# Optimization experiments

Hardware: AMD Instinct MI355X
Metric: run time of the kernel (lower is better)

## Reference

```python
import jax, jax.numpy as jnp
import numpy as np

EMBED = 512
HEADS = 8
SEQ = 2048
HD = EMBED // HEADS  # 64
N_BATCH = 2


def setup_inputs() -> dict:
    key = jax.random.key(0)
    ks = jax.random.split(key, 15)
    f = jax.random.normal
    return {
        "v": f(ks[0], (N_BATCH, SEQ, EMBED), jnp.float32),
        "k": f(ks[1], (N_BATCH, SEQ, EMBED), jnp.float32),
        "q": f(ks[2], (N_BATCH, SEQ, EMBED), jnp.float32),
        # per-head Linear(head_dim, head_dim) weights (stored torch-style [out,in]) + biases
        "Wv": f(ks[3], (HD, HD), jnp.float32) * (HD ** -0.5),
        "bv": f(ks[4], (HD,), jnp.float32) * 0.01,
        "Wk": f(ks[5], (HD, HD), jnp.float32) * (HD ** -0.5),
        "bk": f(ks[6], (HD,), jnp.float32) * 0.01,
        "Wq": f(ks[7], (HD, HD), jnp.float32) * (HD ** -0.5),
        "bq": f(ks[8], (HD,), jnp.float32) * 0.01,
        # relative position embedding E: [1, seq_len, head_dim]
        "E": f(ks[9], (1, SEQ, HD), jnp.float32),
        # fc_out Linear(embed, embed)
        "Wo": f(ks[10], (EMBED, EMBED), jnp.float32) * (EMBED ** -0.5),
        "bo": f(ks[11], (EMBED,), jnp.float32) * 0.01,
    }


def reference(v, k, q, Wv, bv, Wk, bk, Wq, bq, E, Wo, bo):
    N, S, Emb = v.shape
    H = HEADS
    Hd = Emb // H
    # split heads then per-head projections (Linear acts on last dim head_dim)
    values = v.reshape(N, S, H, Hd) @ Wv.T + bv   # [N,S,H,Hd]
    keys = k.reshape(N, S, H, Hd) @ Wk.T + bk
    queries = q.reshape(N, S, H, Hd) @ Wq.T + bq

    # --- Music-Transformer relative-position skew ---
    # QE = queries.transpose(1,2) @ E.transpose(1,2): [N,H,S,Hd] x [Hd,S] -> [N,H,S,S]
    QE = jnp.einsum('nshd,ld->nhsl', queries, E[0])
    triu1 = jnp.triu(jnp.ones((S, S), dtype=jnp.float32), 1)
    pos_mask = jnp.flip(triu1, axis=1)            # triu(...,1).flip(1)
    QE = jnp.where(pos_mask == 1, 0.0, QE)        # _mask_positions
    padded = jnp.pad(QE, ((0, 0), (0, 0), (0, 0), (1, 0)))  # F.pad(qe, [1,0])
    Srel = padded.reshape(N, H, S + 1, S)[:, :, 1:, :]       # _skew -> [N,H,S,S]

    # --- scores + mask (faithful to original: masked_fill(mask==0, -1e20)
    # i.e. lower triangle incl. diagonal gets -1e20) ---
    qk = jnp.einsum('nqhd,nkhd->nhqk', queries, keys)
    qk = jnp.where(triu1[None, None] == 0, jnp.float32(-1e20), qk)

    # note: scaled by sqrt(embed_size), as in the source
    attention = jax.nn.softmax(qk / jnp.sqrt(jnp.float32(Emb)), axis=3) + Srel

    z = jnp.einsum('nhql,nlhd->nqhd', attention, values).reshape(N, S, H * Hd)
    return z @ Wo.T + bo
```

## Files before the change

kernel.cpp:

```cpp
#include <hip/hip_runtime.h>
#include <hip/hip_bf16.h>

#define SEQLEN 2048
#define NHEADS 8
#define HD 64
#define EMB 512
#define NB 2
#define ST 72

typedef __attribute__((ext_vector_type(8))) short bf16x8;
typedef __attribute__((ext_vector_type(4))) float f32x4;

#define SCALE 0.04419417382415922f
#define NEGS  (-4.4194173824159216e18f)

__device__ __forceinline__ ushort f2b(float f) {
    __hip_bfloat16 h = __float2bfloat16(f);
    return *reinterpret_cast<ushort*>(&h);
}
__device__ __forceinline__ float b2f(ushort u) {
    unsigned int v = ((unsigned int)u) << 16;
    return __builtin_bit_cast(float, v);
}
__device__ __forceinline__ uint4 pack8(float4 a, float4 b) {
    union { ushort u[8]; uint4 v; } r;
    r.u[0] = f2b(a.x); r.u[1] = f2b(a.y); r.u[2] = f2b(a.z); r.u[3] = f2b(a.w);
    r.u[4] = f2b(b.x); r.u[5] = f2b(b.y); r.u[6] = f2b(b.z); r.u[7] = f2b(b.w);
    return r.v;
}

__global__ __launch_bounds__(256, 4) void proj_mfma(
    const float* __restrict__ q, const float* __restrict__ k, const float* __restrict__ v,
    const float* __restrict__ Wq, const float* __restrict__ bq,
    const float* __restrict__ Wk, const float* __restrict__ bk,
    const float* __restrict__ Wv, const float* __restrict__ bv,
    ushort* __restrict__ Qh, ushort* __restrict__ Kh, ushort* __restrict__ VT)
{
    const int mat = blockIdx.z;
    const float* x; const float* W; const float* b;
    switch (mat) {
      case 0:  x = q; W = Wq; b = bq; break;
      case 1:  x = k; W = Wk; b = bk; break;
      default: x = v; W = Wv; b = bv; break;
    }
    __shared__ alignas(16) ushort At[64 * ST];
    __shared__ alignas(16) ushort Bt[64 * ST];
    __shared__ alignas(16) ushort Ct[64 * ST];

    const int tid = threadIdx.x;
    const int w = tid >> 6, l = tid & 63;
    const int l15 = l & 15, l16 = l >> 4;
    const int h  = blockIdx.y;
    const int m0 = blockIdx.x * 64;
    const int n  = m0 / SEQLEN;
    const int s0 = m0 - n * SEQLEN;
    const int wm = (w >> 1) * 32, wn = (w & 1) * 32;
    const int r8 = tid >> 3, ch8 = (tid & 7) * 8;

    {
        const float* xr0 = x + (size_t)(m0 + r8) * EMB + h * HD + ch8;
        const float* xr1 = x + (size_t)(m0 + r8 + 32) * EMB + h * HD + ch8;
        float4 a0 = *(const float4*)xr0, a1 = *(const float4*)(xr0 + 4);
        float4 a2 = *(const float4*)xr1, a3 = *(const float4*)(xr1 + 4);
        const float* wr0 = W + r8 * HD + ch8;
        const float* wr1 = W + (r8 + 32) * HD + ch8;
        float4 b0 = *(const float4*)wr0, b1 = *(const float4*)(wr0 + 4);
        float4 b2 = *(const float4*)wr1, b3 = *(const float4*)(wr1 + 4);
        *(uint4*)&At[r8 * ST + ch8]        = pack8(a0, a1);
        *(uint4*)&At[(r8 + 32) * ST + ch8] = pack8(a2, a3);
        *(uint4*)&Bt[r8 * ST + ch8]        = pack8(b0, b1);
        *(uint4*)&Bt[(r8 + 32) * ST + ch8] = pack8(b2, b3);
    }
    __syncthreads();

    f32x4 acc[2][2];
    #pragma unroll
    for (int i = 0; i < 2; ++i)
        #pragma unroll
        for (int j = 0; j < 2; ++j) acc[i][j] = (f32x4){0.f, 0.f, 0.f, 0.f};

    #pragma unroll
    for (int ks = 0; ks < 2; ++ks) {
        const int ko = ks * 32 + l16 * 8;
        bf16x8 af[2], bf[2];
        #pragma unroll
        for (int i = 0; i < 2; ++i) {
            af[i] = *(const bf16x8*)&At[(wm + i * 16 + l15) * ST + ko];
            bf[i] = *(const bf16x8*)&Bt[(wn + i * 16 + l15) * ST + ko];
        }
        #pragma unroll
        for (int i = 0; i < 2; ++i)
            #pragma unroll
            for (int j = 0; j < 2; ++j)
                acc[i][j] = __builtin_amdgcn_mfma_f32_16x16x32_bf16(af[i], bf[j], acc[i][j], 0, 0, 0);
    }

    float bb[2];
    #pragma unroll
    for (int j = 0; j < 2; ++j) bb[j] = b[wn + j * 16 + l15];
    #pragma unroll
    for (int i = 0; i < 2; ++i)
        #pragma unroll
        for (int j = 0; j < 2; ++j)
            #pragma unroll
            for (int r = 0; r < 4; ++r) {
                const int srow = wm + i * 16 + l16 * 4 + r;
                const int dcol = wn + j * 16 + l15;
                const ushort val = f2b(acc[i][j][r] + bb[j]);
                if (mat < 2) Ct[srow * ST + dcol] = val;
                else         Ct[dcol * ST + srow] = val;
            }
    __syncthreads();

    const size_t hb = ((size_t)(n * NHEADS + h)) * SEQLEN * HD;
    if (mat < 2) {
        ushort* dst = (mat == 0 ? Qh : Kh);
        *(uint4*)(dst + hb + (size_t)(s0 + r8) * HD + ch8)      = *(uint4*)&Ct[r8 * ST + ch8];
        *(uint4*)(dst + hb + (size_t)(s0 + r8 + 32) * HD + ch8) = *(uint4*)&Ct[(r8 + 32) * ST + ch8];
    } else {
        *(uint4*)(VT + hb + (size_t)r8 * SEQLEN + s0 + ch8)        = *(uint4*)&Ct[r8 * ST + ch8];
        *(uint4*)(VT + hb + (size_t)(r8 + 32) * SEQLEN + s0 + ch8) = *(uint4*)&Ct[(r8 + 32) * ST + ch8];
    }
}

__global__ __launch_bounds__(256) void econv_kernel(
    const float* __restrict__ E, ushort* __restrict__ Eb)
{
    const int i = (blockIdx.x * 256 + threadIdx.x) * 4;
    float4 f = *(const float4*)(E + i);
    ushort4 u;
    u.x = f2b(f.x); u.y = f2b(f.y); u.z = f2b(f.z); u.w = f2b(f.w);
    *(ushort4*)(Eb + i) = u;
}

__global__ __launch_bounds__(256, 2) void attn_mfma(
    const ushort* __restrict__ Qh, const ushort* __restrict__ Kh,
    const ushort* __restrict__ VT, const ushort* __restrict__ Eb,
    ushort* __restrict__ Z)
{
    const int q0 = blockIdx.x * 64;
    const int h = blockIdx.y, n = blockIdx.z;
    const int tid = threadIdx.x;
    const int w = tid >> 6;
    const int l = tid & 63;
    const int l15 = l & 15, l16 = l >> 4;

    __shared__ alignas(16) ushort Kt[64 * ST];
    __shared__ alignas(16) ushort Vt[64 * ST];
    __shared__ alignas(16) ushort Et[128 * ST];
    __shared__ alignas(16) ushort Wt[4][16 * ST];
    __shared__ float vpart[4][64];
    __shared__ float vsum[64];

    const size_t hb = ((size_t)(n * NHEADS + h)) * SEQLEN * HD;
    const bool lastBlk = (q0 == SEQLEN - 64);
    const int qw = q0 + 16 * w;

    bf16x8 qa[2];
    {
        const ushort* qp = Qh + hb + (size_t)(qw + l15) * HD + l16 * 8;
        qa[0] = *(const bf16x8*)(qp);
        qa[1] = *(const bf16x8*)(qp + 32);
    }

    f32x4 zp[4], zr[4];
    #pragma unroll
    for (int nb = 0; nb < 4; ++nb) {
        zp[nb] = (f32x4){0.f, 0.f, 0.f, 0.f};
        zr[nb] = (f32x4){0.f, 0.f, 0.f, 0.f};
    }
    float mrow[4], lrow[4];
    #pragma unroll
    for (int r = 0; r < 4; ++r) { mrow[r] = NEGS; lrow[r] = 0.f; }
    float vloc = 0.f;

    for (int t = 0; t < 32; ++t) {
        const int c0 = t * 64;
        const bool hasP = (c0 >= q0);
        const bool hasR = (c0 <= q0);
        const bool diag = (c0 == q0);

        __syncthreads();
        {
            const int r8 = tid >> 3;
            const int ch8 = (tid & 7) * 8;
            uint4 v0 = *(const uint4*)(VT + hb + (size_t)r8 * SEQLEN + c0 + ch8);
            uint4 v1 = *(const uint4*)(VT + hb + (size_t)(r8 + 32) * SEQLEN + c0 + ch8);
            uint4 k0, k1;
            if (hasP) {
                k0 = *(const uint4*)(Kh + hb + (size_t)(c0 + r8) * HD + ch8);
                k1 = *(const uint4*)(Kh + hb + (size_t)(c0 + r8 + 32) * HD + ch8);
            }
            uint4 e[4];
            int jmin = 0;
            if (hasR) {
                jmin = SEQLEN - 64 - q0 + c0;
                #pragma unroll
                for (int i = 0; i < 4; ++i) {
                    const int j = jmin + r8 + 32 * i;
                    if (j < SEQLEN) e[i] = *(const uint4*)(Eb + (size_t)j * HD + ch8);
                    else e[i] = make_uint4(0u, 0u, 0u, 0u);
                }
            }
            *(uint4*)&Vt[r8 * ST + ch8] = v0;
            *(uint4*)&Vt[(r8 + 32) * ST + ch8] = v1;
            if (hasP) {
                *(uint4*)&Kt[r8 * ST + ch8] = k0;
                *(uint4*)&Kt[(r8 + 32) * ST + ch8] = k1;
            }
            if (hasR) {
                #pragma unroll
                for (int i = 0; i < 4; ++i)
                    *(uint4*)&Et[(r8 + 32 * i) * ST + ch8] = e[i];
            }
        }
        __syncthreads();

        if (lastBlk) {
            const uint4 a = *(const uint4*)&Vt[l * ST + 16 * w];
            const uint4 b = *(const uint4*)&Vt[l * ST + 16 * w + 8];
            const ushort* pa = (const ushort*)&a;
            const ushort* pb = (const ushort*)&b;
            #pragma unroll
            for (int i = 0; i < 8; ++i) vloc += b2f(pa[i]) + b2f(pb[i]);
        }

        if (hasP) {
            f32x4 sc[4];
            #pragma unroll
            for (int nb = 0; nb < 4; ++nb) sc[nb] = (f32x4){0.f, 0.f, 0.f, 0.f};
            #pragma unroll
            for (int ks = 0; ks < 2; ++ks) {
                const int ko = ks * 32 + l16 * 8;
                #pragma unroll
                for (int nb = 0; nb < 4; ++nb) {
                    bf16x8 kb = *(const bf16x8*)&Kt[(nb * 16 + l15) * ST + ko];
                    sc[nb] = __builtin_amdgcn_mfma_f32_16x16x32_bf16(qa[ks], kb, sc[nb], 0, 0, 0);
                }
            }
            float sv[4][4], mt[4], frs[4];
            #pragma unroll
            for (int r = 0; r < 4; ++r) mt[r] = NEGS;
            #pragma unroll
            for (int nb = 0; nb < 4; ++nb)
                #pragma unroll
                for (int r = 0; r < 4; ++r) {
                    float s = sc[nb][r] * SCALE;
                    if (diag && (nb * 16 + l15 <= 16 * w + l16 * 4 + r)) s = NEGS;
                    sv[nb][r] = s;
                    mt[r] = fmaxf(mt[r], s);
                }
            #pragma unroll
            for (int r = 0; r < 4; ++r) {
                #pragma unroll
                for (int off = 1; off < 16; off <<= 1)
                    mt[r] = fmaxf(mt[r], __shfl_xor(mt[r], off, 64));
                const float mn = fmaxf(mrow[r], mt[r]);
                frs[r] = __expf(mrow[r] - mn);
                mrow[r] = mn;
                lrow[r] *= frs[r];
            }
            float se[4] = {0.f, 0.f, 0.f, 0.f};
            #pragma unroll
            for (int nb = 0; nb < 4; ++nb)
                #pragma unroll
                for (int r = 0; r < 4; ++r) {
                    const float e = __expf(sv[nb][r] - mrow[r]);
                    se[r] += e;
                    Wt[w][(l16 * 4 + r) * ST + nb * 16 + l15] = f2b(e);
                }
            #pragma unroll
            for (int r = 0; r < 4; ++r) {
                #pragma unroll
                for (int off = 1; off < 16; off <<= 1)
                    se[r] += __shfl_xor(se[r], off, 64);
                lrow[r] += se[r];
            }
            #pragma unroll
            for (int nb = 0; nb < 4; ++nb)
                #pragma unroll
                for (int r = 0; r < 4; ++r) zp[nb][r] *= frs[r];
            #pragma unroll
            for (int ks = 0; ks < 2; ++ks) {
                const int ko = ks * 32 + l16 * 8;
                bf16x8 wa = *(const bf16x8*)&Wt[w][l15 * ST + ko];
                #pragma unroll
                for (int nb = 0; nb < 4; ++nb) {
                    bf16x8 vb = *(const bf16x8*)&Vt[(nb * 16 + l15) * ST + ko];
                    zp[nb] = __builtin_amdgcn_mfma_f32_16x16x32_bf16(wa, vb, zp[nb], 0, 0, 0);
                }
            }
        }

        if (hasR) {
            const int jbase = 48 - 16 * w;
            f32x4 qe[5];
            #pragma unroll
            for (int jb = 0; jb < 5; ++jb) qe[jb] = (f32x4){0.f, 0.f, 0.f, 0.f};
            #pragma unroll
            for (int ks = 0; ks < 2; ++ks) {
                const int ko = ks * 32 + l16 * 8;
                #pragma unroll
                for (int jb = 0; jb < 5; ++jb) {
                    bf16x8 eb = *(const bf16x8*)&Et[(jbase + jb * 16 + l15) * ST + ko];
                    qe[jb] = __builtin_amdgcn_mfma_f32_16x16x32_bf16(qa[ks], eb, qe[jb], 0, 0, 0);
                }
            }
            #pragma unroll
            for (int jb = 0; jb < 5; ++jb)
                #pragma unroll
                for (int r = 0; r < 4; ++r) {
                    const int rowloc = l16 * 4 + r;
                    const int cloc = jb * 16 + l15 + rowloc - 15;
                    if (cloc >= 0 && cloc < 64) {
                        const bool msk = (c0 + cloc <= qw + rowloc);
                        Wt[w][rowloc * ST + cloc] = f2b(msk ? qe[jb][r] : 0.f);
                    }
                }
            #pragma unroll
            for (int ks = 0; ks < 2; ++ks) {
                const int ko = ks * 32 + l16 * 8;
                bf16x8 wa = *(const bf16x8*)&Wt[w][l15 * ST + ko];
                #pragma unroll
                for (int nb = 0; nb < 4; ++nb) {
                    bf16x8 vb = *(const bf16x8*)&Vt[(nb * 16 + l15) * ST + ko];
                    zr[nb] = __builtin_amdgcn_mfma_f32_16x16x32_bf16(wa, vb, zr[nb], 0, 0, 0);
                }
            }
        }
    }

    if (lastBlk) vpart[w][l] = vloc;
    __syncthreads();
    if (lastBlk && tid < 64)
        vsum[tid] = vpart[0][tid] + vpart[1][tid] + vpart[2][tid] + vpart[3][tid];
    __syncthreads();

    float invl[4];
    #pragma unroll
    for (int r = 0; r < 4; ++r) invl[r] = 1.f / lrow[r];
    #pragma unroll
    for (int nb = 0; nb < 4; ++nb)
        #pragma unroll
        for (int r = 0; r < 4; ++r) {
            const int q = qw + l16 * 4 + r;
            const int d = nb * 16 + l15;
            float z = zp[nb][r] * invl[r] + zr[nb][r];
            if (lastBlk && q == SEQLEN - 1)
                z = vsum[d] * (1.f / (float)SEQLEN) + zr[nb][r];
            Z[((size_t)(n * SEQLEN + q)) * EMB + h * HD + d] = f2b(z);
        }
}

__global__ __launch_bounds__(256, 4) void oproj_mfma(
    const ushort* __restrict__ Zb, const ushort* __restrict__ Wob,
    const float* __restrict__ bo, float* __restrict__ out)
{
    __shared__ alignas(16) ushort At[64 * ST];
    __shared__ alignas(16) ushort Bt[64 * ST];
    const int tid = threadIdx.x;
    const int w = tid >> 6, l = tid & 63;
    const int l15 = l & 15, l16 = l >> 4;
    const int m0 = blockIdx.x * 64;
    const int n0 = blockIdx.y * 64;
    const int wm = (w >> 1) * 32, wn = (w & 1) * 32;
    const int r8 = tid >> 3, ch8 = (tid & 7) * 8;

    f32x4 acc[2][2];
    #pragma unroll
    for (int i = 0; i < 2; ++i)
        #pragma unroll
        for (int j = 0; j < 2; ++j) acc[i][j] = (f32x4){0.f, 0.f, 0.f, 0.f};

    for (int kt = 0; kt < 8; ++kt) {
        const int k0 = kt * 64;
        __syncthreads();
        {
            uint4 a0 = *(const uint4*)(Zb  + (size_t)(m0 + r8) * EMB + k0 + ch8);
            uint4 a1 = *(const uint4*)(Zb  + (size_t)(m0 + r8 + 32) * EMB + k0 + ch8);
            uint4 b0 = *(const uint4*)(Wob + (size_t)(n0 + r8) * EMB + k0 + ch8);
            uint4 b1 = *(const uint4*)(Wob + (size_t)(n0 + r8 + 32) * EMB + k0 + ch8);
            *(uint4*)&At[r8 * ST + ch8] = a0;
            *(uint4*)&At[(r8 + 32) * ST + ch8] = a1;
            *(uint4*)&Bt[r8 * ST + ch8] = b0;
            *(uint4*)&Bt[(r8 + 32) * ST + ch8] = b1;
        }
        __syncthreads();
        #pragma unroll
        for (int ks = 0; ks < 2; ++ks) {
            const int ko = ks * 32 + l16 * 8;
            bf16x8 af[2], bf[2];
            #pragma unroll
            for (int i = 0; i < 2; ++i) {
                af[i] = *(const bf16x8*)&At[(wm + i * 16 + l15) * ST + ko];
                bf[i] = *(const bf16x8*)&Bt[(wn + i * 16 + l15) * ST + ko];
            }
            #pragma unroll
            for (int i = 0; i < 2; ++i)
                #pragma unroll
                for (int j = 0; j < 2; ++j)
                    acc[i][j] = __builtin_amdgcn_mfma_f32_16x16x32_bf16(af[i], bf[j], acc[i][j], 0, 0, 0);
        }
    }

    #pragma unroll
    for (int i = 0; i < 2; ++i)
        #pragma unroll
        for (int j = 0; j < 2; ++j) {
            const int o = n0 + wn + j * 16 + l15;
            const float bb = bo[o];
            #pragma unroll
            for (int r = 0; r < 4; ++r) {
                const int t = m0 + wm + i * 16 + l16 * 4 + r;
                out[(size_t)t * EMB + o] = acc[i][j][r] + bb;
            }
        }
}

extern "C" void kernel_launch(void* const* d_in, const int* in_sizes, int n_in,
                              void* d_out, int out_size, void* d_ws, size_t ws_size,
                              hipStream_t stream) {
    const float* v  = (const float*)d_in[0];
    const float* k  = (const float*)d_in[1];
    const float* q  = (const float*)d_in[2];
    const float* Wv = (const float*)d_in[3];
    const float* bv = (const float*)d_in[4];
    const float* Wk = (const float*)d_in[5];
    const float* bk = (const float*)d_in[6];
    const float* Wq = (const float*)d_in[7];
    const float* bq = (const float*)d_in[8];
    const float* E  = (const float*)d_in[9];
    const float* Wo = (const float*)d_in[10];
    const float* bo = (const float*)d_in[11];
    float* out = (float*)d_out;

    ushort* wsu = (ushort*)d_ws;
    const size_t perE = (size_t)NB * NHEADS * SEQLEN * HD;
    ushort* Qh  = wsu;
    ushort* Kh  = wsu + perE;
    ushort* VT  = wsu + 2 * perE;
    ushort* Eb  = wsu + 3 * perE;
    ushort* Wob = wsu + 3 * perE + 131072;
    ushort* Zb  = wsu + 3 * perE + 131072 + 262144;

    dim3 gp(NB * SEQLEN / 64, NHEADS, 3);
    proj_mfma<<<gp, 256, 0, stream>>>(q, k, v, Wq, bq, Wk, bk, Wv, bv, Qh, Kh, VT);

    econv_kernel<<<SEQLEN * HD / (256 * 4), 256, 0, stream>>>(E, Eb);
    econv_kernel<<<EMB * EMB / (256 * 4), 256, 0, stream>>>(Wo, Wob);

    dim3 g2(SEQLEN / 64, NHEADS, NB);
    attn_mfma<<<g2, 256, 0, stream>>>(Qh, Kh, VT, Eb, Zb);

    dim3 g3(NB * SEQLEN / 64, EMB / 64);
    oproj_mfma<<<g3, 256, 0, stream>>>(Zb, Wob, bo, out);
}
```

Before: 174.3 us.

## Split key tiles across waves per 16-query block with cross-wave softmax merge

Each attention block now handles 16 query rows instead of 64, and its four waves stride over key tiles (split-K) instead of each owning 16 queries. K, V and E fragments are read straight from global memory into registers, replacing the shared-memory staging and the per-tile barriers. Partial softmax states (max, sum, partial outputs in bf16) are merged across waves through LDS at the end. The last-row V mean moves to a separate small vsum kernel. This gives four times more blocks and removes the synchronisation, but drops reuse of each K/V tile across four query groups, so global and L2 traffic rises, and the partial outputs are rounded to bf16 before the merge.

```diff
diff --git a/kernel.cpp b/kernel.cpp
--- a/kernel.cpp
+++ b/kernel.cpp
@@ -7,6 +7,7 @@
 #define EMB 512
 #define NB 2
 #define ST 72
+#define ZST 66
 
 typedef __attribute__((ext_vector_type(8))) short bf16x8;
 typedef __attribute__((ext_vector_type(4))) float f32x4;
@@ -133,32 +134,48 @@
     *(ushort4*)(Eb + i) = u;
 }
 
-__global__ __launch_bounds__(256, 2) void attn_mfma(
+__global__ __launch_bounds__(256) void vsum_kernel(
+    const ushort* __restrict__ VT, float* __restrict__ vsumG)
+{
+    const int nh = blockIdx.x;
+    const int tid = threadIdx.x;
+    const int d = tid >> 2, part = tid & 3;
+    const ushort* p = VT + (size_t)nh * SEQLEN * HD + (size_t)d * SEQLEN + part * 512;
+    float s = 0.f;
+    for (int i = 0; i < 64; ++i) {
+        uint4 u = *(const uint4*)(p + i * 8);
+        const ushort* pu = (const ushort*)&u;
+        #pragma unroll
+        for (int j = 0; j < 8; ++j) s += b2f(pu[j]);
+    }
+    __shared__ float red[64][4];
+    red[d][part] = s;
+    __syncthreads();
+    if (tid < 64)
+        vsumG[nh * HD + tid] = red[tid][0] + red[tid][1] + red[tid][2] + red[tid][3];
+}
+
+__global__ __launch_bounds__(256, 4) void attn_mfma(
     const ushort* __restrict__ Qh, const ushort* __restrict__ Kh,
     const ushort* __restrict__ VT, const ushort* __restrict__ Eb,
-    ushort* __restrict__ Z)
+    const float* __restrict__ vsumG, ushort* __restrict__ Z)
 {
-    const int q0 = blockIdx.x * 64;
+    const int q0 = blockIdx.x * 16;
     const int h = blockIdx.y, n = blockIdx.z;
     const int tid = threadIdx.x;
-    const int w = tid >> 6;
-    const int l = tid & 63;
+    const int w = tid >> 6, l = tid & 63;
     const int l15 = l & 15, l16 = l >> 4;
 
-    __shared__ alignas(16) ushort Kt[64 * ST];
-    __shared__ alignas(16) ushort Vt[64 * ST];
-    __shared__ alignas(16) ushort Et[128 * ST];
     __shared__ alignas(16) ushort Wt[4][16 * ST];
-    __shared__ float vpart[4][64];
-    __shared__ float vsum[64];
+    __shared__ alignas(16) ushort zpL[4][16 * ZST];
+    __shared__ alignas(16) ushort zrL[4][16 * ZST];
+    __shared__ float mL[4][16], lL[4][16];
 
     const size_t hb = ((size_t)(n * NHEADS + h)) * SEQLEN * HD;
-    const bool lastBlk = (q0 == SEQLEN - 64);
-    const int qw = q0 + 16 * w;
 
     bf16x8 qa[2];
     {
-        const ushort* qp = Qh + hb + (size_t)(qw + l15) * HD + l16 * 8;
+        const ushort* qp = Qh + hb + (size_t)(q0 + l15) * HD + l16 * 8;
         qa[0] = *(const bf16x8*)(qp);
         qa[1] = *(const bf16x8*)(qp + 32);
     }
@@ -172,72 +189,35 @@
     float mrow[4], lrow[4];
     #pragma unroll
     for (int r = 0; r < 4; ++r) { mrow[r] = NEGS; lrow[r] = 0.f; }
-    float vloc = 0.f;
-
-    for (int t = 0; t < 32; ++t) {
+
+    for (int t = w; t < 32; t += 4) {
         const int c0 = t * 64;
-        const bool hasP = (c0 >= q0);
+        const bool hasP = (c0 + 63 > q0);
         const bool hasR = (c0 <= q0);
-        const bool diag = (c0 == q0);
-
-        __syncthreads();
-        {
-            const int r8 = tid >> 3;
-            const int ch8 = (tid & 7) * 8;
-            uint4 v0 = *(const uint4*)(VT + hb + (size_t)r8 * SEQLEN + c0 + ch8);
-            uint4 v1 = *(const uint4*)(VT + hb + (size_t)(r8 + 32) * SEQLEN + c0 + ch8);
-            uint4 k0, k1;
-            if (hasP) {
-                k0 = *(const uint4*)(Kh + hb + (size_t)(c0 + r8) * HD + ch8);
-                k1 = *(const uint4*)(Kh + hb + (size_t)(c0 + r8 + 32) * HD + ch8);
-            }
-            uint4 e[4];
-            int jmin = 0;
-            if (hasR) {
-                jmin = SEQLEN - 64 - q0 + c0;
-                #pragma unroll
-                for (int i = 0; i < 4; ++i) {
-                    const int j = jmin + r8 + 32 * i;
-                    if (j < SEQLEN) e[i] = *(const uint4*)(Eb + (size_t)j * HD + ch8);
-                    else e[i] = make_uint4(0u, 0u, 0u, 0u);
-                }
-            }
-            *(uint4*)&Vt[r8 * ST + ch8] = v0;
-            *(uint4*)&Vt[(r8 + 32) * ST + ch8] = v1;
-            if (hasP) {
-                *(uint4*)&Kt[r8 * ST + ch8] = k0;
-                *(uint4*)&Kt[(r8 + 32) * ST + ch8] = k1;
-            }
-            if (hasR) {
-                #pragma unroll
-                for (int i = 0; i < 4; ++i)
-                    *(uint4*)&Et[(r8 + 32 * i) * ST + ch8] = e[i];
-            }
-        }
-        __syncthreads();
-
-        if (lastBlk) {
-            const uint4 a = *(const uint4*)&Vt[l * ST + 16 * w];
-            const uint4 b = *(const uint4*)&Vt[l * ST + 16 * w + 8];
-            const ushort* pa = (const ushort*)&a;
-            const ushort* pb = (const ushort*)&b;
-            #pragma unroll
-            for (int i = 0; i < 8; ++i) vloc += b2f(pa[i]) + b2f(pb[i]);
-        }
 
         if (hasP) {
+            bf16x8 kb[2][4];
+            #pragma unroll
+            for (int ks = 0; ks < 2; ++ks)
+                #pragma unroll
+                for (int nb = 0; nb < 4; ++nb)
+                    kb[ks][nb] = *(const bf16x8*)(Kh + hb + (size_t)(c0 + nb * 16 + l15) * HD + ks * 32 + l16 * 8);
             f32x4 sc[4];
             #pragma unroll
             for (int nb = 0; nb < 4; ++nb) sc[nb] = (f32x4){0.f, 0.f, 0.f, 0.f};
             #pragma unroll
-            for (int ks = 0; ks < 2; ++ks) {
-                const int ko = ks * 32 + l16 * 8;
-                #pragma unroll
-                for (int nb = 0; nb < 4; ++nb) {
-                    bf16x8 kb = *(const bf16x8*)&Kt[(nb * 16 + l15) * ST + ko];
-                    sc[nb] = __builtin_amdgcn_mfma_f32_16x16x32_bf16(qa[ks], kb, sc[nb], 0, 0, 0);
-                }
-            }
+            for (int ks = 0; ks < 2; ++ks)
+                #pragma unroll
+                for (int nb = 0; nb < 4; ++nb)
+                    sc[nb] = __builtin_amdgcn_mfma_f32_16x16x32_bf16(qa[ks], kb[ks][nb], sc[nb], 0, 0, 0);
+
+            bf16x8 vb[2][4];
+            #pragma unroll
+            for (int ks = 0; ks < 2; ++ks)
+                #pragma unroll
+                for (int nb = 0; nb < 4; ++nb)
+                    vb[ks][nb] = *(const bf16x8*)(VT + hb + (size_t)(nb * 16 + l15) * SEQLEN + c0 + ks * 32 + l16 * 8);
+
             float sv[4][4], mt[4], frs[4];
             #pragma unroll
             for (int r = 0; r < 4; ++r) mt[r] = NEGS;
@@ -246,7 +226,7 @@
                 #pragma unroll
                 for (int r = 0; r < 4; ++r) {
                     float s = sc[nb][r] * SCALE;
-                    if (diag && (nb * 16 + l15 <= 16 * w + l16 * 4 + r)) s = NEGS;
+                    if (c0 + nb * 16 + l15 <= q0 + l16 * 4 + r) s = NEGS;
                     sv[nb][r] = s;
                     mt[r] = fmaxf(mt[r], s);
                 }
@@ -282,30 +262,34 @@
                 for (int r = 0; r < 4; ++r) zp[nb][r] *= frs[r];
             #pragma unroll
             for (int ks = 0; ks < 2; ++ks) {
-                const int ko = ks * 32 + l16 * 8;
-                bf16x8 wa = *(const bf16x8*)&Wt[w][l15 * ST + ko];
-                #pragma unroll
-                for (int nb = 0; nb < 4; ++nb) {
-                    bf16x8 vb = *(const bf16x8*)&Vt[(nb * 16 + l15) * ST + ko];
-                    zp[nb] = __builtin_amdgcn_mfma_f32_16x16x32_bf16(wa, vb, zp[nb], 0, 0, 0);
-                }
+                bf16x8 wa = *(const bf16x8*)&Wt[w][l15 * ST + ks * 32 + l16 * 8];
+                #pragma unroll
+                for (int nb = 0; nb < 4; ++nb)
+                    zp[nb] = __builtin_amdgcn_mfma_f32_16x16x32_bf16(wa, vb[ks][nb], zp[nb], 0, 0, 0);
             }
         }
 
         if (hasR) {
-            const int jbase = 48 - 16 * w;
+            const int jmin = SEQLEN - 16 - q0 + c0;
             f32x4 qe[5];
             #pragma unroll
             for (int jb = 0; jb < 5; ++jb) qe[jb] = (f32x4){0.f, 0.f, 0.f, 0.f};
             #pragma unroll
-            for (int ks = 0; ks < 2; ++ks) {
-                const int ko = ks * 32 + l16 * 8;
+            for (int ks = 0; ks < 2; ++ks)
                 #pragma unroll
                 for (int jb = 0; jb < 5; ++jb) {
-                    bf16x8 eb = *(const bf16x8*)&Et[(jbase + jb * 16 + l15) * ST + ko];
+                    const int j = jmin + jb * 16 + l15;
+                    bf16x8 eb;
+                    if (j < SEQLEN) eb = *(const bf16x8*)(Eb + (size_t)j * HD + ks * 32 + l16 * 8);
+                    else            eb = (bf16x8){0, 0, 0, 0, 0, 0, 0, 0};
                     qe[jb] = __builtin_amdgcn_mfma_f32_16x16x32_bf16(qa[ks], eb, qe[jb], 0, 0, 0);
                 }
-            }
+            bf16x8 vb[2][4];
+            #pragma unroll
+            for (int ks = 0; ks < 2; ++ks)
+                #pragma unroll
+                for (int nb = 0; nb < 4; ++nb)
+                    vb[ks][nb] = *(const bf16x8*)(VT + hb + (size_t)(nb * 16 + l15) * SEQLEN + c0 + ks * 32 + l16 * 8);
             #pragma unroll
             for (int jb = 0; jb < 5; ++jb)
                 #pragma unroll
@@ -313,43 +297,59 @@
                     const int rowloc = l16 * 4 + r;
                     const int cloc = jb * 16 + l15 + rowloc - 15;
                     if (cloc >= 0 && cloc < 64) {
-                        const bool msk = (c0 + cloc <= qw + rowloc);
+                        const bool msk = (c0 + cloc <= q0 + rowloc);
                         Wt[w][rowloc * ST + cloc] = f2b(msk ? qe[jb][r] : 0.f);
                     }
                 }
             #pragma unroll
             for (int ks = 0; ks < 2; ++ks) {
-                const int ko = ks * 32 + l16 * 8;
-                bf16x8 wa = *(const bf16x8*)&Wt[w][l15 * ST + ko];
-                #pragma unroll
-                for (int nb = 0; nb < 4; ++nb) {
-                    bf16x8 vb = *(const bf16x8*)&Vt[(nb * 16 + l15) * ST + ko];
-                    zr[nb] = __builtin_amdgcn_mfma_f32_16x16x32_bf16(wa, vb, zr[nb], 0, 0, 0);
-                }
-            }
-        }
-    }
-
-    if (lastBlk) vpart[w][l] = vloc;
+                bf16x8 wa = *(const bf16x8*)&Wt[w][l15 * ST + ks * 32 + l16 * 8];
+                #pragma unroll
+                for (int nb = 0; nb < 4; ++nb)
+                    zr[nb] = __builtin_amdgcn_mfma_f32_16x16x32_bf16(wa, vb[ks][nb], zr[nb], 0, 0, 0);
+            }
+        }
+    }
+
+    #pragma unroll
+    for (int nb = 0; nb < 4; ++nb)
+        #pragma unroll
+        for (int r = 0; r < 4; ++r) {
+            const int row = l16 * 4 + r;
+            zpL[w][row * ZST + nb * 16 + l15] = f2b(zp[nb][r]);
+            zrL[w][row * ZST + nb * 16 + l15] = f2b(zr[nb][r]);
+        }
+    if (l15 == 0) {
+        #pragma unroll
+        for (int r = 0; r < 4; ++r) {
+            mL[w][l16 * 4 + r] = mrow[r];
+            lL[w][l16 * 4 + r] = lrow[r];
+        }
+    }
     __syncthreads();
-    if (lastBlk && tid < 64)
-        vsum[tid] = vpart[0][tid] + vpart[1][tid] + vpart[2][tid] + vpart[3][tid];
-    __syncthreads();
-
-    float invl[4];
-    #pragma unroll
-    for (int r = 0; r < 4; ++r) invl[r] = 1.f / lrow[r];
-    #pragma unroll
-    for (int nb = 0; nb < 4; ++nb)
-        #pragma unroll
-        for (int r = 0; r < 4; ++r) {
-            const int q = qw + l16 * 4 + r;
-            const int d = nb * 16 + l15;
-            float z = zp[nb][r] * invl[r] + zr[nb][r];
-            if (lastBlk && q == SEQLEN - 1)
-                z = vsum[d] * (1.f / (float)SEQLEN) + zr[nb][r];
-            Z[((size_t)(n * SEQLEN + q)) * EMB + h * HD + d] = f2b(z);
-        }
+
+    const int d = tid & 63, g = tid >> 6;
+    #pragma unroll
+    for (int i = 0; i < 4; ++i) {
+        const int row = g * 4 + i;
+        const float M = fmaxf(fmaxf(mL[0][row], mL[1][row]), fmaxf(mL[2][row], mL[3][row]));
+        float ew[4], L = 0.f;
+        #pragma unroll
+        for (int w2 = 0; w2 < 4; ++w2) {
+            ew[w2] = __expf(mL[w2][row] - M);
+            L += lL[w2][row] * ew[w2];
+        }
+        float zps = 0.f, zrs = 0.f;
+        #pragma unroll
+        for (int w2 = 0; w2 < 4; ++w2) {
+            zps += b2f(zpL[w2][row * ZST + d]) * ew[w2];
+            zrs += b2f(zrL[w2][row * ZST + d]);
+        }
+        float z = zps / L + zrs;
+        if (q0 + row == SEQLEN - 1)
+            z = vsumG[(n * NHEADS + h) * HD + d] * (1.f / (float)SEQLEN) + zrs;
+        Z[((size_t)(n * SEQLEN + q0 + row)) * EMB + h * HD + d] = f2b(z);
+    }
 }
 
 __global__ __launch_bounds__(256, 4) void oproj_mfma(
@@ -442,6 +442,7 @@
     ushort* Eb  = wsu + 3 * perE;
     ushort* Wob = wsu + 3 * perE + 131072;
     ushort* Zb  = wsu + 3 * perE + 131072 + 262144;
+    float*  vsumG = (float*)(Zb + perE);
 
     dim3 gp(NB * SEQLEN / 64, NHEADS, 3);
     proj_mfma<<<gp, 256, 0, stream>>>(q, k, v, Wq, bq, Wk, bk, Wv, bv, Qh, Kh, VT);
@@ -449,8 +450,10 @@
     econv_kernel<<<SEQLEN * HD / (256 * 4), 256, 0, stream>>>(E, Eb);
     econv_kernel<<<EMB * EMB / (256 * 4), 256, 0, stream>>>(Wo, Wob);
 
-    dim3 g2(SEQLEN / 64, NHEADS, NB);
-    attn_mfma<<<g2, 256, 0, stream>>>(Qh, Kh, VT, Eb, Zb);
+    vsum_kernel<<<NB * NHEADS, 256, 0, stream>>>(VT, vsumG);
+
+    dim3 g2(SEQLEN / 16, NHEADS, NB);
+    attn_mfma<<<g2, 256, 0, stream>>>(Qh, Kh, VT, Eb, vsumG, Zb);
 
     dim3 g3(NB * SEQLEN / 64, EMB / 64);
     oproj_mfma<<<g3, 256, 0, stream>>>(Zb, Wob, bo, out);
```

New measurement: 272.6 us. +56.4%, slower.
